# Optimization experiments

Hardware: AMD Instinct MI355X
Metric: run time of the kernel (lower is better)

## Reference

```python
import jax, jax.numpy as jnp
import numpy as np
from jax import lax

B, C, H, W = 32, 256, 64, 64
MCH = 16   # max(8, 256//16)
KS = 5     # ECA 1D kernel: int((log2(256)+1)/2)=4 -> odd-adjust 5
EPS = 1e-5

def setup_inputs() -> dict:
    key = jax.random.key(0)
    ks = jax.random.split(key, 9)
    return {
        "x": jax.random.normal(ks[0], (B, C, H, W), jnp.float32),
        "w10": jax.random.normal(ks[1], (MCH, C), jnp.float32) * 0.05,   # 1x1 conv C->MCH
        "w11": jax.random.normal(ks[2], (C, MCH), jnp.float32) * 0.05,   # 1x1 conv MCH->C
        "bn_gamma": jax.random.normal(ks[3], (MCH,), jnp.float32) * 0.1 + 1.0,
        "bn_beta": jax.random.normal(ks[4], (MCH,), jnp.float32) * 0.1,
        "bn_mean": jax.random.normal(ks[5], (MCH,), jnp.float32) * 0.1,
        "bn_var": jax.random.uniform(ks[6], (MCH,), jnp.float32, 0.5, 1.5),
        "w20": jax.random.normal(ks[7], (KS,), jnp.float32) * 0.2,       # 1D ECA kernel
        "w21": jax.random.normal(ks[8], (1, 1, 3, 3), jnp.float32) * 0.2,  # spatial 3x3
    }

def reference(x, w10, w11, bn_gamma, bn_beta, bn_mean, bn_var, w20, w21):
    b, c, h, w = x.shape
    # --- channel (ECA) branch: global avg pool -> 1D conv over channel dim ---
    pooled = jnp.mean(x, axis=(2, 3))                      # [b, c]
    f_ch = lax.conv_general_dilated(
        pooled[:, None, :], w20[None, None, :], (1,), 'SAME',
        dimension_numbers=('NCH', 'OIH', 'NCH'))[:, 0, :]   # [b, c]
    f_ch = f_ch[:, :, None, None]                           # [b, c, 1, 1] (no sigmoid, as in source)
    # --- spatial branch: channel mean -> 3x3 conv -> sigmoid ---
    f_sa = jax.nn.sigmoid(lax.conv_general_dilated(
        jnp.mean(x, axis=1, keepdims=True), w21, (1, 1), 'SAME',
        dimension_numbers=('NCHW', 'OIHW', 'NCHW')))        # [b, 1, h, w]
    # --- coordinate branch ---
    x_h = jnp.mean(x, axis=3)                               # [b, c, h]
    x_w = jnp.mean(x, axis=2)                               # [b, c, w]
    cat = jnp.concatenate([x_h, x_w], axis=2)               # [b, c, h+w]
    y = jnp.einsum('mc,bcl->bml', w10, cat)                 # 1x1 conv
    inv = lax.rsqrt(bn_var + EPS) * bn_gamma                # BN (inference)
    y = jax.nn.relu(y * inv[None, :, None] + (bn_beta - bn_mean * inv)[None, :, None])
    yh, yw = y[:, :, :h], y[:, :, h:]
    s_h = jax.nn.sigmoid(jnp.einsum('cm,bmh->bch', w11, yh))[:, :, :, None]  # [b,c,h,1]
    s_w = jax.nn.sigmoid(jnp.einsum('cm,bmw->bcw', w11, yw))[:, :, None, :]  # [b,c,1,w]
    F = f_ch + s_h * s_w + f_sa
    return x * F
```

## Files before the change

kernel.cpp:

```cpp
#include <hip/hip_runtime.h>
#include <hip/hip_bf16.h>

#define NB 32
#define NC 256
#define NH 64
#define NW 64

typedef unsigned short u16;

__device__ int   g_mode;
__device__ float g_cmeanp[NB * 16 * 4096];
__device__ float g_yp[NB * 16 * 16 * 128];
__device__ float g_pooled[NB * NC];
__device__ float g_fch[NB * NC];
__device__ float g_fsa[NB * 4096];
__device__ float g_sh[NB * NC * 64];
__device__ float g_sw[NB * NC * 64];

__device__ __forceinline__ float bf2f(unsigned int u) {
    union { unsigned int i; float f; } v; v.i = u << 16; return v.f;
}
__device__ __forceinline__ u16 f2bf(float f) {
    union { float f; unsigned int i; } v; v.f = f;
    unsigned int i = v.i;
    unsigned int r = (i + 0x7fffu + ((i >> 16) & 1u)) >> 16;
    return (u16)r;
}
__device__ __forceinline__ unsigned int pack2(float a, float b) {
    return (unsigned int)f2bf(a) | ((unsigned int)f2bf(b) << 16);
}
__device__ __forceinline__ float sigmoidf_(float x) {
    return 1.f / (1.f + expf(-x));
}

__device__ __forceinline__ void loadx8(const void* x, size_t i8, int mode, float* v) {
    if (mode) {
        const uint4 u = ((const uint4*)x)[i8];
        v[0] = bf2f(u.x & 0xffffu); v[1] = bf2f(u.x >> 16);
        v[2] = bf2f(u.y & 0xffffu); v[3] = bf2f(u.y >> 16);
        v[4] = bf2f(u.z & 0xffffu); v[5] = bf2f(u.z >> 16);
        v[6] = bf2f(u.w & 0xffffu); v[7] = bf2f(u.w >> 16);
    } else {
        const float4 a = ((const float4*)x)[i8 * 2];
        const float4 b = ((const float4*)x)[i8 * 2 + 1];
        v[0] = a.x; v[1] = a.y; v[2] = a.z; v[3] = a.w;
        v[4] = b.x; v[5] = b.y; v[6] = b.z; v[7] = b.w;
    }
}
__device__ __forceinline__ float loadw(const void* p, int i, int mode) {
    return mode ? bf2f((unsigned int)((const u16*)p)[i]) : ((const float*)p)[i];
}
__device__ __forceinline__ void store8(void* o, size_t i8, int mode, const float* v) {
    if (mode) {
        uint4 u;
        u.x = pack2(v[0], v[1]);
        u.y = pack2(v[2], v[3]);
        u.z = pack2(v[4], v[5]);
        u.w = pack2(v[6], v[7]);
        ((uint4*)o)[i8] = u;
    } else {
        ((float4*)o)[i8 * 2]     = make_float4(v[0], v[1], v[2], v[3]);
        ((float4*)o)[i8 * 2 + 1] = make_float4(v[4], v[5], v[6], v[7]);
    }
}

__global__ __launch_bounds__(256) void kA(const void* __restrict__ x,
                                          const void* __restrict__ w10) {
    __shared__ unsigned int sliceP[4][2048];
    __shared__ float rowsum[16 * 64];
    __shared__ float colsum[16 * 64];
    __shared__ float w10s[256];
    __shared__ int scnt;

    const int t  = threadIdx.x;
    const int ln = t & 63, wv = t >> 6;
    const int cg = blockIdx.x;
    const int b  = blockIdx.y;

    if (t == 0) scnt = 0;
    __syncthreads();
    {
        const u16* xr = (const u16*)x;
        int local = 0;
#pragma unroll
        for (int i = 0; i < 8; ++i) {
            const u16 w = xr[(t * 8 + i) * 2];
            const unsigned e = (w >> 7) & 0xffu;
            if (w == 0 || (e >= 0x40u && e <= 0x90u)) ++local;
        }
        atomicAdd(&scnt, local);
    }
    __syncthreads();
    const int mode = (scnt >= 1536) ? 1 : 0;
    if ((blockIdx.x | blockIdx.y) == 0 && t == 0) g_mode = mode;

    w10s[t] = loadw(w10, (t >> 4) * NC + cg * 16 + (t & 15), mode);

    float colacc[4][8];
#pragma unroll
    for (int cc = 0; cc < 4; ++cc)
#pragma unroll
        for (int k = 0; k < 8; ++k) colacc[cc][k] = 0.f;

    const int ch0 = cg * 16 + wv * 4;
    const size_t i8base = (((size_t)(b * NC + ch0)) << 9) + ln;

    for (int p = 0; p < 8; ++p) {
        float cme[8];
#pragma unroll
        for (int k = 0; k < 8; ++k) cme[k] = 0.f;
#pragma unroll
        for (int cc = 0; cc < 4; ++cc) {
            float v[8];
            loadx8(x, i8base + (((size_t)cc) << 9) + p * 64, mode, v);
#pragma unroll
            for (int k = 0; k < 8; ++k) {
                cme[k] += v[k];
                colacc[cc][k] += v[k];
            }
            float s = ((v[0] + v[1]) + (v[2] + v[3])) + ((v[4] + v[5]) + (v[6] + v[7]));
            s += __shfl_xor(s, 1);
            s += __shfl_xor(s, 2);
            s += __shfl_xor(s, 4);
            if ((ln & 7) == 0)
                rowsum[(wv * 4 + cc) * 64 + p * 8 + (ln >> 3)] = s;
        }
        uint4 pk;
        pk.x = pack2(cme[0], cme[1]);
        pk.y = pack2(cme[2], cme[3]);
        pk.z = pack2(cme[4], cme[5]);
        pk.w = pack2(cme[6], cme[7]);
        *(uint4*)&sliceP[wv][p * 256 + ln * 4] = pk;
    }

#pragma unroll
    for (int cc = 0; cc < 4; ++cc)
#pragma unroll
        for (int k = 0; k < 8; ++k) {
            float v = colacc[cc][k];
            v += __shfl_xor(v, 8);
            v += __shfl_xor(v, 16);
            v += __shfl_xor(v, 32);
            colacc[cc][k] = v;
        }
    if (ln < 8) {
#pragma unroll
        for (int cc = 0; cc < 4; ++cc) {
            *(float4*)&colsum[(wv * 4 + cc) * 64 + ln * 8] =
                make_float4(colacc[cc][0], colacc[cc][1], colacc[cc][2], colacc[cc][3]);
            *(float4*)&colsum[(wv * 4 + cc) * 64 + ln * 8 + 4] =
                make_float4(colacc[cc][4], colacc[cc][5], colacc[cc][6], colacc[cc][7]);
        }
    }
    __syncthreads();

    {
        const int u0 = t * 8;
        float acc[16];
#pragma unroll
        for (int k = 0; k < 16; ++k) acc[k] = 0.f;
#pragma unroll
        for (int w = 0; w < 4; ++w) {
            const uint4 qa = *(const uint4*)&sliceP[w][u0];
            const uint4 qb = *(const uint4*)&sliceP[w][u0 + 4];
            const unsigned int uu[8] = {qa.x, qa.y, qa.z, qa.w, qb.x, qb.y, qb.z, qb.w};
#pragma unroll
            for (int k = 0; k < 8; ++k) {
                acc[2 * k]     += bf2f(uu[k] & 0xffffu);
                acc[2 * k + 1] += bf2f(uu[k] >> 16);
            }
        }
        const float invC = 1.f / 256.f;
        float* dst = g_cmeanp + (((size_t)(b * 16 + cg)) << 12) + t * 16;
#pragma unroll
        for (int k4 = 0; k4 < 4; ++k4)
            *(float4*)(dst + k4 * 4) = make_float4(acc[k4 * 4] * invC,
                                                   acc[k4 * 4 + 1] * invC,
                                                   acc[k4 * 4 + 2] * invC,
                                                   acc[k4 * 4 + 3] * invC);
    }

    {
        const int lc = t >> 4, j = t & 15;
        const float* rs = rowsum + lc * 64 + j * 4;
        float s = (rs[0] + rs[1]) + (rs[2] + rs[3]);
        s += __shfl_xor(s, 1);
        s += __shfl_xor(s, 2);
        s += __shfl_xor(s, 4);
        s += __shfl_xor(s, 8);
        if (j == 0) g_pooled[b * NC + cg * 16 + lc] = s * (1.f / 4096.f);
    }

    {
        const int m = t >> 4, l0 = (t & 15) * 8;
        const float* base = (l0 < 64) ? (rowsum + l0) : (colsum + l0 - 64);
        float acc[8];
#pragma unroll
        for (int k = 0; k < 8; ++k) acc[k] = 0.f;
#pragma unroll
        for (int lc = 0; lc < 16; ++lc) {
            const float wvv = w10s[m * 16 + lc];
            const float4 s0 = *(const float4*)(base + lc * 64);
            const float4 s1 = *(const float4*)(base + lc * 64 + 4);
            acc[0] = fmaf(wvv, s0.x, acc[0]);
            acc[1] = fmaf(wvv, s0.y, acc[1]);
            acc[2] = fmaf(wvv, s0.z, acc[2]);
            acc[3] = fmaf(wvv, s0.w, acc[3]);
            acc[4] = fmaf(wvv, s1.x, acc[4]);
            acc[5] = fmaf(wvv, s1.y, acc[5]);
            acc[6] = fmaf(wvv, s1.z, acc[6]);
            acc[7] = fmaf(wvv, s1.w, acc[7]);
        }
        const float inv64 = 1.f / 64.f;
        float* dst = g_yp + ((((size_t)b * 16 + cg) * 16 + m) << 7) + l0;
        *(float4*)dst =
            make_float4(acc[0] * inv64, acc[1] * inv64, acc[2] * inv64, acc[3] * inv64);
        *(float4*)(dst + 4) =
            make_float4(acc[4] * inv64, acc[5] * inv64, acc[6] * inv64, acc[7] * inv64);
    }
}

__global__ __launch_bounds__(256) void kB(
    const void* __restrict__ w11,
    const void* __restrict__ bn_gamma, const void* __restrict__ bn_beta,
    const void* __restrict__ bn_mean, const void* __restrict__ bn_var,
    const void* __restrict__ w20, const void* __restrict__ w21) {

    __shared__ float w11_lds[2048];
    __shared__ float y_lds[16 * 65];
    __shared__ float cm[18 * 64];
    __shared__ float pooled[260];
    __shared__ float bnA[16], bnBv[16];

    const int t  = threadIdx.x;
    const int bx = blockIdx.x;
    const int half = bx >> 1, csplit = bx & 1;
    const int b  = blockIdx.y;
    const int mode = g_mode;

    for (int j = t; j < 2048; j += 256)
        w11_lds[j] = loadw(w11, csplit * 2048 + j, mode);
    if (t < 16) {
        const float inv = rsqrtf(loadw(bn_var, t, mode) + 1e-5f) *
                          loadw(bn_gamma, t, mode);
        bnA[t]  = inv;
        bnBv[t] = loadw(bn_beta, t, mode) - loadw(bn_mean, t, mode) * inv;
    }
    __syncthreads();

    {
        const int l = t & 63;
        const float* src0 = g_yp + ((size_t)b << 15) + half * 64 + l;
#pragma unroll
        for (int r = 0; r < 4; ++r) {
            const int m = r * 4 + (t >> 6);
            const float* src = src0 + m * 128;
            float s = 0.f;
#pragma unroll
            for (int cgi = 0; cgi < 16; ++cgi)
                s += src[cgi * 2048];
            y_lds[m * 65 + l] = fmaxf(fmaf(s, bnA[m], bnBv[m]), 0.f);
        }
    }
    __syncthreads();

    {
        const int h = t & 63, q = t >> 6;
        float yr[16];
#pragma unroll
        for (int mm = 0; mm < 16; ++mm) yr[mm] = y_lds[mm * 65 + h];
        float* sout = half ? g_sw : g_sh;
        const size_t sb = ((size_t)b) * NC * 64;
        for (int ci = 0; ci < 32; ++ci) {
            const int cl = q * 32 + ci;
            const float4* wrow = (const float4*)(w11_lds + cl * 16);
            const float4 w0 = wrow[0], w1 = wrow[1], w2 = wrow[2], w3 = wrow[3];
            float acc;
            acc = fmaf(w0.x, yr[0], w0.y * yr[1]);
            acc = fmaf(w0.z, yr[2], acc); acc = fmaf(w0.w, yr[3], acc);
            acc = fmaf(w1.x, yr[4], acc); acc = fmaf(w1.y, yr[5], acc);
            acc = fmaf(w1.z, yr[6], acc); acc = fmaf(w1.w, yr[7], acc);
            acc = fmaf(w2.x, yr[8], acc); acc = fmaf(w2.y, yr[9], acc);
            acc = fmaf(w2.z, yr[10], acc); acc = fmaf(w2.w, yr[11], acc);
            acc = fmaf(w3.x, yr[12], acc); acc = fmaf(w3.y, yr[13], acc);
            acc = fmaf(w3.z, yr[14], acc); acc = fmaf(w3.w, yr[15], acc);
            sout[sb + (size_t)(csplit * 128 + cl) * 64 + h] = sigmoidf_(acc);
        }
    }

    {
        const int r0 = bx * 16;
        const int c0 = (r0 == 0) ? 0 : (r0 - 1);
        const int c1 = (r0 + 16 > 63) ? 63 : (r0 + 16);
        const int n  = (c1 - c0 + 1) * 64;
        const float* srcb = g_cmeanp + (((size_t)b * 16) << 12) + c0 * 64;
        for (int j = t; j < n; j += 256) {
            float s = 0.f;
#pragma unroll
            for (int gcg = 0; gcg < 16; ++gcg)
                s += srcb[((size_t)gcg << 12) + j];
            cm[j] = s;
        }
        __syncthreads();
        float w21f[9];
#pragma unroll
        for (int k = 0; k < 9; ++k) w21f[k] = loadw(w21, k, mode);
#pragma unroll
        for (int rr = 0; rr < 4; ++rr) {
            const int j  = rr * 256 + t;
            const int hh = r0 + (j >> 6), ww = j & 63;
            float acc = 0.f;
#pragma unroll
            for (int dy = 0; dy < 3; ++dy) {
                const int hy = hh + dy - 1;
                if (hy < 0 || hy > 63) continue;
#pragma unroll
                for (int dx = 0; dx < 3; ++dx) {
                    const int wx = ww + dx - 1;
                    if (wx < 0 || wx > 63) continue;
                    acc = fmaf(w21f[dy * 3 + dx], cm[(hy - c0) * 64 + wx], acc);
                }
            }
            g_fsa[b * 4096 + hh * 64 + ww] = sigmoidf_(acc);
        }
    }

    if (bx == 0) {
        pooled[2 + t] = g_pooled[b * NC + t];
        if (t < 2) { pooled[t] = 0.f; pooled[258 + t] = 0.f; }
        __syncthreads();
        float w20f[5];
#pragma unroll
        for (int k = 0; k < 5; ++k) w20f[k] = loadw(w20, k, mode);
        float acc = 0.f;
#pragma unroll
        for (int k = 0; k < 5; ++k) acc = fmaf(w20f[k], pooled[t + k], acc);
        g_fch[b * NC + t] = acc;
    }
}

__global__ __launch_bounds__(256) void kC(const void* __restrict__ x,
                                          void* __restrict__ out) {
    const unsigned e = blockIdx.x * 256 + threadIdx.x;
    const int w0 = (e & 7) << 3;
    const int h  = (e >> 3) & 63;
    const int c  = (e >> 9) & 255;
    const int b  = e >> 17;
    const int mode = g_mode;

    float v[8];
    loadx8(x, e, mode, v);

    const float fc = g_fch[b * NC + c];
    const float sh = g_sh[((size_t)(b * NC + c)) * 64 + h];
    const float* swp = g_sw + ((size_t)(b * NC + c)) * 64 + w0;
    const float* fsp = g_fsa + (size_t)b * 4096 + h * 64 + w0;
    const float4 swa = *(const float4*)(swp);
    const float4 swb = *(const float4*)(swp + 4);
    const float4 fsa = *(const float4*)(fsp);
    const float4 fsb = *(const float4*)(fsp + 4);

    float r[8];
    r[0] = v[0] * (fc + sh * swa.x + fsa.x);
    r[1] = v[1] * (fc + sh * swa.y + fsa.y);
    r[2] = v[2] * (fc + sh * swa.z + fsa.z);
    r[3] = v[3] * (fc + sh * swa.w + fsa.w);
    r[4] = v[4] * (fc + sh * swb.x + fsb.x);
    r[5] = v[5] * (fc + sh * swb.y + fsb.y);
    r[6] = v[6] * (fc + sh * swb.z + fsb.z);
    r[7] = v[7] * (fc + sh * swb.w + fsb.w);

    store8(out, e, mode, r);
}

extern "C" void kernel_launch(void* const* d_in, const int* in_sizes, int n_in,
                              void* d_out, int out_size, void* d_ws, size_t ws_size,
                              hipStream_t stream) {
    const void* x        = d_in[0];
    const void* w10      = d_in[1];
    const void* w11      = d_in[2];
    const void* bn_gamma = d_in[3];
    const void* bn_beta  = d_in[4];
    const void* bn_mean  = d_in[5];
    const void* bn_var   = d_in[6];
    const void* w20      = d_in[7];
    const void* w21      = d_in[8];

    kA<<<dim3(16, NB), 256, 0, stream>>>(x, w10);
    kB<<<dim3(4, NB), 256, 0, stream>>>(w11, bn_gamma, bn_beta,
                                        bn_mean, bn_var, w20, w21);
    kC<<<(NB * NC * NH * NW / 8) / 256, 256, 0, stream>>>(x, d_out);
}
```

Baseline: 290.2 us.

## Store channel-mean partials as bf16 and split kB across twice as many blocks

kA now writes its per-channel-group channel-mean partials as packed bf16 pairs instead of fp32, which halves that intermediate buffer's write and read traffic. kB is relaunched with 8 blocks per batch instead of 4. Each block now handles a quarter of the w11 channels and 8 rows of the spatial conv, so the small middle kernel has more parallelism. The cost is reduced precision in the spatial-branch channel mean, which is accumulated from bf16 values, and more redundant halo loads and repeated w11/BN setup across blocks.

```diff
diff --git a/kernel.cpp b/kernel.cpp
--- a/kernel.cpp
+++ b/kernel.cpp
@@ -9,7 +9,7 @@
 typedef unsigned short u16;
 
 __device__ int   g_mode;
-__device__ float g_cmeanp[NB * 16 * 4096];
+__device__ unsigned int g_cmeanpU[NB * 16 * 2048];
 __device__ float g_yp[NB * 16 * 16 * 128];
 __device__ float g_pooled[NB * NC];
 __device__ float g_fch[NB * NC];
@@ -171,13 +171,13 @@
             }
         }
         const float invC = 1.f / 256.f;
-        float* dst = g_cmeanp + (((size_t)(b * 16 + cg)) << 12) + t * 16;
-#pragma unroll
-        for (int k4 = 0; k4 < 4; ++k4)
-            *(float4*)(dst + k4 * 4) = make_float4(acc[k4 * 4] * invC,
-                                                   acc[k4 * 4 + 1] * invC,
-                                                   acc[k4 * 4 + 2] * invC,
-                                                   acc[k4 * 4 + 3] * invC);
+        unsigned int pk[8];
+#pragma unroll
+        for (int k = 0; k < 8; ++k)
+            pk[k] = pack2(acc[2 * k] * invC, acc[2 * k + 1] * invC);
+        unsigned int* dst = g_cmeanpU + (((size_t)(b * 16 + cg)) << 11) + t * 8;
+        *(uint4*)dst       = make_uint4(pk[0], pk[1], pk[2], pk[3]);
+        *(uint4*)(dst + 4) = make_uint4(pk[4], pk[5], pk[6], pk[7]);
     }
 
     {
@@ -226,20 +226,20 @@
     const void* __restrict__ bn_mean, const void* __restrict__ bn_var,
     const void* __restrict__ w20, const void* __restrict__ w21) {
 
-    __shared__ float w11_lds[2048];
+    __shared__ float w11_lds[1024];
     __shared__ float y_lds[16 * 65];
-    __shared__ float cm[18 * 64];
+    __shared__ float cm[10 * 64];
     __shared__ float pooled[260];
     __shared__ float bnA[16], bnBv[16];
 
     const int t  = threadIdx.x;
     const int bx = blockIdx.x;
-    const int half = bx >> 1, csplit = bx & 1;
+    const int half = bx >> 2, quarter = bx & 3;
     const int b  = blockIdx.y;
     const int mode = g_mode;
 
-    for (int j = t; j < 2048; j += 256)
-        w11_lds[j] = loadw(w11, csplit * 2048 + j, mode);
+    for (int j = t; j < 1024; j += 256)
+        w11_lds[j] = loadw(w11, quarter * 1024 + j, mode);
     if (t < 16) {
         const float inv = rsqrtf(loadw(bn_var, t, mode) + 1e-5f) *
                           loadw(bn_gamma, t, mode);
@@ -271,8 +271,8 @@
         for (int mm = 0; mm < 16; ++mm) yr[mm] = y_lds[mm * 65 + h];
         float* sout = half ? g_sw : g_sh;
         const size_t sb = ((size_t)b) * NC * 64;
-        for (int ci = 0; ci < 32; ++ci) {
-            const int cl = q * 32 + ci;
+        for (int ci = 0; ci < 16; ++ci) {
+            const int cl = q * 16 + ci;
             const float4* wrow = (const float4*)(w11_lds + cl * 16);
             const float4 w0 = wrow[0], w1 = wrow[1], w2 = wrow[2], w3 = wrow[3];
             float acc;
@@ -284,29 +284,34 @@
             acc = fmaf(w2.z, yr[10], acc); acc = fmaf(w2.w, yr[11], acc);
             acc = fmaf(w3.x, yr[12], acc); acc = fmaf(w3.y, yr[13], acc);
             acc = fmaf(w3.z, yr[14], acc); acc = fmaf(w3.w, yr[15], acc);
-            sout[sb + (size_t)(csplit * 128 + cl) * 64 + h] = sigmoidf_(acc);
-        }
-    }
-
-    {
-        const int r0 = bx * 16;
+            sout[sb + (size_t)(quarter * 64 + cl) * 64 + h] = sigmoidf_(acc);
+        }
+    }
+
+    {
+        const int r0 = bx * 8;
         const int c0 = (r0 == 0) ? 0 : (r0 - 1);
-        const int c1 = (r0 + 16 > 63) ? 63 : (r0 + 16);
-        const int n  = (c1 - c0 + 1) * 64;
-        const float* srcb = g_cmeanp + (((size_t)b * 16) << 12) + c0 * 64;
-        for (int j = t; j < n; j += 256) {
-            float s = 0.f;
-#pragma unroll
-            for (int gcg = 0; gcg < 16; ++gcg)
-                s += srcb[((size_t)gcg << 12) + j];
-            cm[j] = s;
+        const int c1 = (r0 + 8 > 63) ? 63 : (r0 + 8);
+        const int nu = (c1 - c0 + 1) * 32;
+        const unsigned int* srcb =
+            g_cmeanpU + (((size_t)b * 16) << 11) + c0 * 32;
+        for (int j = t; j < nu; j += 256) {
+            float s0 = 0.f, s1 = 0.f;
+#pragma unroll
+            for (int gcg = 0; gcg < 16; ++gcg) {
+                const unsigned int u = srcb[((size_t)gcg << 11) + j];
+                s0 += bf2f(u & 0xffffu);
+                s1 += bf2f(u >> 16);
+            }
+            cm[2 * j]     = s0;
+            cm[2 * j + 1] = s1;
         }
         __syncthreads();
         float w21f[9];
 #pragma unroll
         for (int k = 0; k < 9; ++k) w21f[k] = loadw(w21, k, mode);
 #pragma unroll
-        for (int rr = 0; rr < 4; ++rr) {
+        for (int rr = 0; rr < 2; ++rr) {
             const int j  = rr * 256 + t;
             const int hh = r0 + (j >> 6), ww = j & 63;
             float acc = 0.f;
@@ -387,7 +392,7 @@
     const void* w21      = d_in[8];
 
     kA<<<dim3(16, NB), 256, 0, stream>>>(x, w10);
-    kB<<<dim3(4, NB), 256, 0, stream>>>(w11, bn_gamma, bn_beta,
+    kB<<<dim3(8, NB), 256, 0, stream>>>(w11, bn_gamma, bn_beta,
                                         bn_mean, bn_var, w20, w21);
     kC<<<(NB * NC * NH * NW / 8) / 256, 256, 0, stream>>>(x, d_out);
 }
```

Result: no change. 289.0 us (-0.4%).
